# Kernel tuning notes

Measured on AMD Instinct MI355X. Metric: run time of the kernel, lower is better.

The kernel has to match this reference:

```python
import jax, jax.numpy as jnp
import numpy as np

N_OBJ, N_PTS, K_NN = 8, 2048, 10
TOL_CONTACT = 0.01


def setup_inputs() -> dict:
    key = jax.random.key(0)
    k1, k2, k3 = jax.random.split(key, 3)
    # per-object sampled points: xyz + (unit) normals
    pts = jax.random.normal(k1, (N_OBJ, N_PTS, 6), dtype=jnp.float32)
    nrm = pts[..., 3:6]
    nrm = nrm / jnp.linalg.norm(nrm, axis=-1, keepdims=True)
    points = jnp.concatenate([pts[..., :3], nrm], axis=-1)
    # near-identity rigid-ish transforms (keeps inverse well conditioned)
    T_est = jnp.eye(4, dtype=jnp.float32)[None] + 0.05 * jax.random.normal(k2, (N_OBJ, 4, 4), dtype=jnp.float32)
    T_plane = jnp.eye(4, dtype=jnp.float32) + 0.05 * jax.random.normal(k3, (4, 4), dtype=jnp.float32)
    return {"points": points, "T_est": T_est, "T_plane": T_plane, "k": K_NN}


def reference(points, T_est, T_plane, k):
    # points: [N, P, 6] (xyz, normal), T_est: [N, 4, 4], T_plane: [4, 4]
    N = points.shape[0]
    M = jnp.linalg.inv(T_plane) @ T_est                      # [N,4,4]
    xyz = points[..., :3]
    x = jnp.einsum('nij,npj->npi', M[:, :3, :3], xyz) + M[:, None, :3, 3]  # [N,P,3] points in plane frame
    z = x[..., 2]                                            # plane signed distance [N,P]
    nrm = points[..., 3:6]                                   # normals (untransformed, as in source)

    # all-pairs squared distances: d2[b,o,p,q] = ||x[b,p] - x[o,q]||^2
    sq = jnp.sum(x * x, axis=-1)                             # [N,P]
    d2 = sq[:, None, :, None] + sq[None, :, None, :] - 2.0 * jnp.einsum('bpd,oqd->bopq', x, x)
    neg_d2, idx = jax.lax.top_k(-d2, k)                      # [N,N,P,k], nearest k in object o for query (b,p)
    dist = jnp.sqrt(jnp.maximum(-neg_d2, 0.0))               # [N,N,P,k]

    # gather nearest points / normals from source object o
    o_idx = jnp.arange(N)[None, :, None, None]               # broadcast over [N,N,P,k]
    near = x[o_idx, idx]                                     # [N,N,P,k,3]
    near_n = nrm[o_idx, idx]                                 # [N,N,P,k,3]

    grad = near - x[:, None, :, None, :]                     # [N,N,P,k,3]
    grad = grad / jnp.linalg.norm(grad, axis=-1, keepdims=True)
    insides = jnp.sum(near_n * grad, axis=-1) > 0            # [N,N,P,k]
    inside = jnp.sum(insides, axis=-1) > k * 0.8             # [N,N,P]

    d0 = dist[..., 0]                                        # nearest distance [N,N,P]
    d0 = jnp.where(inside, -d0, d0)
    self_mask = jnp.eye(N, dtype=bool)[:, :, None]           # exclude o == b
    d0 = jnp.where(self_mask, jnp.inf, d0)
    sd_other = jnp.min(d0, axis=1)                           # [N,P] min over other objects

    signed_distance = jnp.minimum(z, sd_other)               # [N,P]
    intersects = signed_distance < -TOL_CONTACT
    return signed_distance, intersects
```

## Files before the change

kernel.cpp:

```cpp
#include <hip/hip_runtime.h>
#include <cfloat>
#include <math.h>

#define N_OBJ 8
#define N_PTS 2048
#define KNN   10
#define TOLC  0.01f
#define TPB   256
#define NW    4
#define QC    (N_PTS / NW)
#define PC    64
#define NCHUNK (N_PTS / PC)

__device__ __forceinline__ unsigned int enc_f(float f) {
    unsigned int u = __float_as_uint(f);
    return (u & 0x80000000u) ? ~u : (u | 0x80000000u);
}
__device__ __forceinline__ float dec_f(unsigned int e) {
    unsigned int u = (e & 0x80000000u) ? (e & 0x7fffffffu) : ~e;
    return __uint_as_float(u);
}

__global__ void k_transform(const float* __restrict__ pts,
                            const float* __restrict__ T_est,
                            const float* __restrict__ T_plane,
                            float4* __restrict__ P4g,
                            float4* __restrict__ N4g,
                            unsigned int* __restrict__ SD) {
    int gid = blockIdx.x * blockDim.x + threadIdx.x;
    if (gid >= N_OBJ * N_PTS) return;
    int b = gid >> 11;

    double m[16];
#pragma unroll
    for (int i = 0; i < 16; i++) m[i] = (double)T_plane[i];
    double inv[16];
    inv[0]  =  m[5]*m[10]*m[15] - m[5]*m[11]*m[14] - m[9]*m[6]*m[15] + m[9]*m[7]*m[14] + m[13]*m[6]*m[11] - m[13]*m[7]*m[10];
    inv[4]  = -m[4]*m[10]*m[15] + m[4]*m[11]*m[14] + m[8]*m[6]*m[15] - m[8]*m[7]*m[14] - m[12]*m[6]*m[11] + m[12]*m[7]*m[10];
    inv[8]  =  m[4]*m[9]*m[15]  - m[4]*m[11]*m[13] - m[8]*m[5]*m[15] + m[8]*m[7]*m[13] + m[12]*m[5]*m[11] - m[12]*m[7]*m[9];
    inv[12] = -m[4]*m[9]*m[14]  + m[4]*m[10]*m[13] + m[8]*m[5]*m[14] - m[8]*m[6]*m[13] - m[12]*m[5]*m[10] + m[12]*m[6]*m[9];
    inv[1]  = -m[1]*m[10]*m[15] + m[1]*m[11]*m[14] + m[9]*m[2]*m[15] - m[9]*m[3]*m[14] - m[13]*m[2]*m[11] + m[13]*m[3]*m[10];
    inv[5]  =  m[0]*m[10]*m[15] - m[0]*m[11]*m[14] - m[8]*m[2]*m[15] + m[8]*m[3]*m[14] + m[12]*m[2]*m[11] - m[12]*m[3]*m[10];
    inv[9]  = -m[0]*m[9]*m[15]  + m[0]*m[11]*m[13] + m[8]*m[1]*m[15] - m[8]*m[3]*m[13] - m[12]*m[1]*m[11] + m[12]*m[3]*m[9];
    inv[13] =  m[0]*m[9]*m[14]  - m[0]*m[10]*m[13] - m[8]*m[1]*m[14] + m[8]*m[2]*m[13] + m[12]*m[1]*m[10] - m[12]*m[2]*m[9];
    inv[2]  =  m[1]*m[6]*m[15]  - m[1]*m[7]*m[14]  - m[5]*m[2]*m[15] + m[5]*m[3]*m[14] + m[13]*m[2]*m[7]  - m[13]*m[3]*m[6];
    inv[6]  = -m[0]*m[6]*m[15]  + m[0]*m[7]*m[14]  + m[4]*m[2]*m[15] - m[4]*m[3]*m[14] - m[12]*m[2]*m[7]  + m[12]*m[3]*m[6];
    inv[10] =  m[0]*m[5]*m[15]  - m[0]*m[7]*m[13]  - m[4]*m[1]*m[15] + m[4]*m[3]*m[13] + m[12]*m[1]*m[7]  - m[12]*m[3]*m[5];
    inv[14] = -m[0]*m[5]*m[14]  + m[0]*m[6]*m[13]  + m[4]*m[1]*m[14] - m[4]*m[2]*m[13] - m[12]*m[1]*m[6]  + m[12]*m[2]*m[5];
    inv[3]  = -m[1]*m[6]*m[11]  + m[1]*m[7]*m[10]  + m[5]*m[2]*m[11] - m[5]*m[3]*m[10] - m[9]*m[2]*m[7]   + m[9]*m[3]*m[6];
    inv[7]  =  m[0]*m[6]*m[11]  - m[0]*m[7]*m[10]  - m[4]*m[2]*m[11] + m[4]*m[3]*m[10] + m[8]*m[2]*m[7]   - m[8]*m[3]*m[6];
    inv[11] = -m[0]*m[5]*m[11]  + m[0]*m[7]*m[9]   + m[4]*m[1]*m[11] - m[4]*m[3]*m[9]  - m[8]*m[1]*m[7]   + m[8]*m[3]*m[5];
    inv[15] =  m[0]*m[5]*m[10]  - m[0]*m[6]*m[9]   - m[4]*m[1]*m[10] + m[4]*m[2]*m[9]  + m[8]*m[1]*m[6]   - m[8]*m[2]*m[5];
    double det  = m[0]*inv[0] + m[1]*inv[4] + m[2]*inv[8] + m[3]*inv[12];
    double rdet = 1.0 / det;

    const float* Te = T_est + b * 16;
    double M[12];
#pragma unroll
    for (int i = 0; i < 3; i++)
#pragma unroll
        for (int j = 0; j < 4; j++) {
            double s = 0.0;
#pragma unroll
            for (int kk = 0; kk < 4; kk++) s += inv[i*4+kk] * rdet * (double)Te[kk*4+j];
            M[i*4+j] = s;
        }

    const float* pp = pts + (size_t)gid * 6;
    double px = pp[0], py = pp[1], pz = pp[2];
    float nx = pp[3], ny = pp[4], nz = pp[5];
    float x = (float)(M[0]*px + M[1]*py + M[2]*pz  + M[3]);
    float y = (float)(M[4]*px + M[5]*py + M[6]*pz  + M[7]);
    float z = (float)(M[8]*px + M[9]*py + M[10]*pz + M[11]);
    float sq = fmaf(x, x, fmaf(y, y, z * z));
    float w  = fmaf(nx, x, fmaf(ny, y, nz * z));
    P4g[gid] = make_float4(x, y, z, sq);
    N4g[gid] = make_float4(nx, ny, nz, w);
    SD[gid]  = enc_f(z);
}

#define QB(PX,PY,PZ,PW,NX,NY,NZ,NWW) \
  "v_mul_f32 %[t0], " PZ ", %[mz]\n" \
  "v_fma_f32 %[t0], %[my], " PY ", %[t0]\n" \
  "v_fma_f32 %[t0], %[mx], " PX ", %[t0]\n" \
  "v_add_f32 %[t0], " PW ", %[t0]\n" \
  "v_mul_f32 %[t1], " NZ ", %[gz]\n" \
  "v_fma_f32 %[t1], %[gy], " NY ", %[t1]\n" \
  "v_fma_f32 %[t1], %[gx], " NX ", %[t1]\n" \
  "v_add_f32 %[t1], " NWW ", %[t1]\n" \
  "v_and_b32 %[t0], -2, %[t0]\n" \
  "v_cmp_lt_f32 vcc, 0, %[t1]\n" \
  "v_cndmask_b32_e64 %[t1], 0, 1, vcc\n" \
  "v_or_b32 %[t0], %[t0], %[t1]\n" \
  "v_med3_f32 %[d9], %[d8], %[d9], %[t0]\n" \
  "v_med3_f32 %[d8], %[d7], %[d8], %[t0]\n" \
  "v_med3_f32 %[d7], %[d6], %[d7], %[t0]\n" \
  "v_med3_f32 %[d6], %[d5], %[d6], %[t0]\n" \
  "v_med3_f32 %[d5], %[d4], %[d5], %[t0]\n" \
  "v_med3_f32 %[d4], %[d3], %[d4], %[t0]\n" \
  "v_med3_f32 %[d3], %[d2], %[d3], %[t0]\n" \
  "v_med3_f32 %[d2], %[d1], %[d2], %[t0]\n" \
  "v_med3_f32 %[d1], %[d0], %[d1], %[t0]\n" \
  "v_min_f32 %[d0], %[d0], %[t0]\n"

__global__ void __launch_bounds__(TPB, 8) k_pairs(const float4* __restrict__ P4g,
                                                  const float4* __restrict__ N4g,
                                                  unsigned int* __restrict__ SD) {
    __shared__ float MRG[NW][PC][KNN + 1];

    int bx   = blockIdx.x;
    int pair = bx >> 5;
    int c64  = bx & (NCHUNK - 1);
    int b  = pair / 7;
    int oi = pair % 7;
    int o  = oi + (oi >= b ? 1 : 0);
    int tid  = threadIdx.x;
    int lane = tid & 63;
    int wu   = __builtin_amdgcn_readfirstlane(tid >> 6);
    int p    = c64 * PC + lane;

    float4 xp = P4g[b * N_PTS + p];
    float mx = -2.0f * xp.x, my = -2.0f * xp.y, mz = -2.0f * xp.z;
    float gx = -xp.x, gy = -xp.y, gz = -xp.z;

    const float4* Po = P4g + o * N_PTS + wu * QC;
    const float4* No = N4g + o * N_PTS + wu * QC;
    unsigned long long ap = (unsigned long long)(uintptr_t)Po;
    unsigned long long an = (unsigned long long)(uintptr_t)No;
    unsigned int bpl = (unsigned int)ap, bph = (unsigned int)(ap >> 32);
    unsigned int bnl = (unsigned int)an, bnh = (unsigned int)(an >> 32);

    const float FMAXE = __uint_as_float(0x7F7FFFFEu);
    float d0_ = FMAXE, d1_ = FMAXE, d2_ = FMAXE, d3_ = FMAXE, d4_ = FMAXE;
    float d5_ = FMAXE, d6_ = FMAXE, d7_ = FMAXE, d8_ = FMAXE, d9_ = FMAXE;
    float t0, t1;

    asm volatile(
        "s_mov_b32 s32, %[bpl]\n"
        "s_mov_b32 s33, %[bph]\n"
        "s_mov_b32 s34, %[bnl]\n"
        "s_mov_b32 s35, %[bnh]\n"
        "s_load_dwordx16 s[36:51], s[32:33], 0x0\n"
        "s_load_dwordx16 s[52:67], s[34:35], 0x0\n"
        "s_mov_b32 s30, 0\n"
        "Lkp%=:\n"
        "s_waitcnt lgkmcnt(0)\n"
        "s_load_dwordx16 s[68:83], s[32:33], 0x40\n"
        "s_load_dwordx16 s[84:99], s[34:35], 0x40\n"
        QB("s36","s37","s38","s39","s52","s53","s54","s55")
        QB("s40","s41","s42","s43","s56","s57","s58","s59")
        QB("s44","s45","s46","s47","s60","s61","s62","s63")
        QB("s48","s49","s50","s51","s64","s65","s66","s67")
        "s_waitcnt lgkmcnt(0)\n"
        "s_load_dwordx16 s[36:51], s[32:33], 0x80\n"
        "s_load_dwordx16 s[52:67], s[34:35], 0x80\n"
        QB("s68","s69","s70","s71","s84","s85","s86","s87")
        QB("s72","s73","s74","s75","s88","s89","s90","s91")
        QB("s76","s77","s78","s79","s92","s93","s94","s95")
        QB("s80","s81","s82","s83","s96","s97","s98","s99")
        "s_add_u32 s32, s32, 0x80\n"
        "s_addc_u32 s33, s33, 0\n"
        "s_add_u32 s34, s34, 0x80\n"
        "s_addc_u32 s35, s35, 0\n"
        "s_add_u32 s30, s30, 1\n"
        "s_cmp_lt_u32 s30, 64\n"
        "s_cbranch_scc1 Lkp%=\n"
        "s_waitcnt lgkmcnt(0)\n"
        : [d0]"+v"(d0_), [d1]"+v"(d1_), [d2]"+v"(d2_), [d3]"+v"(d3_),
          [d4]"+v"(d4_), [d5]"+v"(d5_), [d6]"+v"(d6_), [d7]"+v"(d7_),
          [d8]"+v"(d8_), [d9]"+v"(d9_), [t0]"=&v"(t0), [t1]"=&v"(t1)
        : [mx]"v"(mx), [my]"v"(my), [mz]"v"(mz),
          [gx]"v"(gx), [gy]"v"(gy), [gz]"v"(gz),
          [bpl]"s"(bpl), [bph]"s"(bph), [bnl]"s"(bnl), [bnh]"s"(bnh)
        : "s30","s31","s32","s33","s34","s35","s36","s37","s38","s39",
          "s40","s41","s42","s43","s44","s45","s46","s47","s48","s49",
          "s50","s51","s52","s53","s54","s55","s56","s57","s58","s59",
          "s60","s61","s62","s63","s64","s65","s66","s67","s68","s69",
          "s70","s71","s72","s73","s74","s75","s76","s77","s78","s79",
          "s80","s81","s82","s83","s84","s85","s86","s87","s88","s89",
          "s90","s91","s92","s93","s94","s95","s96","s97","s98","s99",
          "scc","vcc","memory");

    float td[KNN] = {d0_, d1_, d2_, d3_, d4_, d5_, d6_, d7_, d8_, d9_};

    if (wu > 0) {
#pragma unroll
        for (int j = 0; j < KNN; j++) MRG[wu][lane][j] = td[j];
    }
    __syncthreads();

    if (wu == 0) {
#pragma unroll
        for (int ww = 1; ww < NW; ww++) {
#pragma unroll
            for (int j = 0; j < KNN; j++) {
                float cp = MRG[ww][lane][j];
#pragma unroll
                for (int t = KNN - 1; t >= 1; --t)
                    td[t] = __builtin_amdgcn_fmed3f(td[t - 1], td[t], cp);
                td[0] = fminf(td[0], cp);
            }
        }

        int cnt = 0;
#pragma unroll
        for (int j = 0; j < KNN; j++) cnt += (int)(__float_as_uint(td[j]) & 1u);
        float d2 = __uint_as_float(__float_as_uint(td[0]) & 0xFFFFFFFEu) + xp.w;
        float d0 = sqrtf(fmaxf(d2, 0.0f));
        if (cnt > 8) d0 = -d0;
        atomicMin(&SD[b * N_PTS + p], enc_f(d0));
    }
}

__global__ void k_final(const unsigned int* __restrict__ SD,
                       float* __restrict__ out) {
    int gid = blockIdx.x * blockDim.x + threadIdx.x;
    if (gid >= N_OBJ * N_PTS) return;
    float sd = dec_f(SD[gid]);
    out[gid] = sd;
    out[N_OBJ * N_PTS + gid] = (sd < -TOLC) ? 1.0f : 0.0f;
}

extern "C" void kernel_launch(void* const* d_in, const int* in_sizes, int n_in,
                              void* d_out, int out_size, void* d_ws, size_t ws_size,
                              hipStream_t stream) {
    const float* pts     = (const float*)d_in[0];
    const float* T_est   = (const float*)d_in[1];
    const float* T_plane = (const float*)d_in[2];

    float4*       P4 = (float4*)d_ws;
    float4*       N4 = P4 + N_OBJ * N_PTS;
    unsigned int* SD = (unsigned int*)(N4 + N_OBJ * N_PTS);

    float* out = (float*)d_out;

    k_transform<<<(N_OBJ * N_PTS) / 256, 256, 0, stream>>>(pts, T_est, T_plane, P4, N4, SD);
    k_pairs<<<N_OBJ * (N_OBJ - 1) * NCHUNK, TPB, 0, stream>>>(P4, N4, SD);
    k_final<<<(N_OBJ * N_PTS) / 256, 256, 0, stream>>>(SD, out);
}
```

Baseline: 168.1 us.

## Stream candidate points via vector global loads with triple-buffered VGPR pipeline

Replaces scalar s_load_dwordx16 streaming of candidate points and normals with wave-uniform global_load_dwordx4 into a three-slot VGPR ring. Loads are issued two slots ahead and waited on with vmcnt, so memory latency overlaps the top-k compute. This uses 96 extra VGPRs, so launch bounds drop from 8 to 4 waves per SIMD, trading occupancy for deeper software pipelining and less scalar-cache pressure.

New measurement: 260.2 us. +54.8%, slower.

```diff
diff --git a/kernel.cpp b/kernel.cpp
--- a/kernel.cpp
+++ b/kernel.cpp
@@ -103,7 +103,40 @@
   "v_med3_f32 %[d1], %[d0], %[d1], %[t0]\n" \
   "v_min_f32 %[d0], %[d0], %[t0]\n"
 
-__global__ void __launch_bounds__(TPB, 8) k_pairs(const float4* __restrict__ P4g,
+#define LDSLOT(P0,P1,P2,P3,Q0,Q1,Q2,Q3,O0,O1,O2,O3) \
+  "global_load_dwordx4 " P0 ", %[vz], s[32:33] offset:" O0 "\n" \
+  "global_load_dwordx4 " P1 ", %[vz], s[32:33] offset:" O1 "\n" \
+  "global_load_dwordx4 " P2 ", %[vz], s[32:33] offset:" O2 "\n" \
+  "global_load_dwordx4 " P3 ", %[vz], s[32:33] offset:" O3 "\n" \
+  "global_load_dwordx4 " Q0 ", %[vz], s[34:35] offset:" O0 "\n" \
+  "global_load_dwordx4 " Q1 ", %[vz], s[34:35] offset:" O1 "\n" \
+  "global_load_dwordx4 " Q2 ", %[vz], s[34:35] offset:" O2 "\n" \
+  "global_load_dwordx4 " Q3 ", %[vz], s[34:35] offset:" O3 "\n"
+
+#define SLOT0_LD(O0,O1,O2,O3) LDSLOT("v[32:35]","v[36:39]","v[40:43]","v[44:47]", \
+                                     "v[48:51]","v[52:55]","v[56:59]","v[60:63]",O0,O1,O2,O3)
+#define SLOT1_LD(O0,O1,O2,O3) LDSLOT("v[64:67]","v[68:71]","v[72:75]","v[76:79]", \
+                                     "v[80:83]","v[84:87]","v[88:91]","v[92:95]",O0,O1,O2,O3)
+#define SLOT2_LD(O0,O1,O2,O3) LDSLOT("v[96:99]","v[100:103]","v[104:107]","v[108:111]", \
+                                     "v[112:115]","v[116:119]","v[120:123]","v[124:127]",O0,O1,O2,O3)
+
+#define SLOT0_QB \
+  QB("v32","v33","v34","v35","v48","v49","v50","v51") \
+  QB("v36","v37","v38","v39","v52","v53","v54","v55") \
+  QB("v40","v41","v42","v43","v56","v57","v58","v59") \
+  QB("v44","v45","v46","v47","v60","v61","v62","v63")
+#define SLOT1_QB \
+  QB("v64","v65","v66","v67","v80","v81","v82","v83") \
+  QB("v68","v69","v70","v71","v84","v85","v86","v87") \
+  QB("v72","v73","v74","v75","v88","v89","v90","v91") \
+  QB("v76","v77","v78","v79","v92","v93","v94","v95")
+#define SLOT2_QB \
+  QB("v96","v97","v98","v99","v112","v113","v114","v115") \
+  QB("v100","v101","v102","v103","v116","v117","v118","v119") \
+  QB("v104","v105","v106","v107","v120","v121","v122","v123") \
+  QB("v108","v109","v110","v111","v124","v125","v126","v127")
+
+__global__ void __launch_bounds__(TPB, 4) k_pairs(const float4* __restrict__ P4g,
                                                   const float4* __restrict__ N4g,
                                                   unsigned int* __restrict__ SD) {
     __shared__ float MRG[NW][PC][KNN + 1];
@@ -140,45 +173,50 @@
         "s_mov_b32 s33, %[bph]\n"
         "s_mov_b32 s34, %[bnl]\n"
         "s_mov_b32 s35, %[bnh]\n"
-        "s_load_dwordx16 s[36:51], s[32:33], 0x0\n"
-        "s_load_dwordx16 s[52:67], s[34:35], 0x0\n"
+        SLOT0_LD("0","16","32","48")
+        SLOT1_LD("64","80","96","112")
         "s_mov_b32 s30, 0\n"
         "Lkp%=:\n"
-        "s_waitcnt lgkmcnt(0)\n"
-        "s_load_dwordx16 s[68:83], s[32:33], 0x40\n"
-        "s_load_dwordx16 s[84:99], s[34:35], 0x40\n"
-        QB("s36","s37","s38","s39","s52","s53","s54","s55")
-        QB("s40","s41","s42","s43","s56","s57","s58","s59")
-        QB("s44","s45","s46","s47","s60","s61","s62","s63")
-        QB("s48","s49","s50","s51","s64","s65","s66","s67")
-        "s_waitcnt lgkmcnt(0)\n"
-        "s_load_dwordx16 s[36:51], s[32:33], 0x80\n"
-        "s_load_dwordx16 s[52:67], s[34:35], 0x80\n"
-        QB("s68","s69","s70","s71","s84","s85","s86","s87")
-        QB("s72","s73","s74","s75","s88","s89","s90","s91")
-        QB("s76","s77","s78","s79","s92","s93","s94","s95")
-        QB("s80","s81","s82","s83","s96","s97","s98","s99")
-        "s_add_u32 s32, s32, 0x80\n"
+        SLOT2_LD("128","144","160","176")
+        "s_waitcnt vmcnt(16)\n"
+        SLOT0_QB
+        SLOT0_LD("192","208","224","240")
+        "s_waitcnt vmcnt(16)\n"
+        SLOT1_QB
+        SLOT1_LD("256","272","288","304")
+        "s_waitcnt vmcnt(16)\n"
+        SLOT2_QB
+        "s_add_u32 s32, s32, 0xc0\n"
         "s_addc_u32 s33, s33, 0\n"
-        "s_add_u32 s34, s34, 0x80\n"
+        "s_add_u32 s34, s34, 0xc0\n"
         "s_addc_u32 s35, s35, 0\n"
         "s_add_u32 s30, s30, 1\n"
-        "s_cmp_lt_u32 s30, 64\n"
+        "s_cmp_lt_u32 s30, 42\n"
         "s_cbranch_scc1 Lkp%=\n"
-        "s_waitcnt lgkmcnt(0)\n"
+        "s_waitcnt vmcnt(8)\n"
+        SLOT0_QB
+        "s_waitcnt vmcnt(0)\n"
+        SLOT1_QB
         : [d0]"+v"(d0_), [d1]"+v"(d1_), [d2]"+v"(d2_), [d3]"+v"(d3_),
           [d4]"+v"(d4_), [d5]"+v"(d5_), [d6]"+v"(d6_), [d7]"+v"(d7_),
           [d8]"+v"(d8_), [d9]"+v"(d9_), [t0]"=&v"(t0), [t1]"=&v"(t1)
         : [mx]"v"(mx), [my]"v"(my), [mz]"v"(mz),
           [gx]"v"(gx), [gy]"v"(gy), [gz]"v"(gz),
+          [vz]"v"(0),
           [bpl]"s"(bpl), [bph]"s"(bph), [bnl]"s"(bnl), [bnh]"s"(bnh)
-        : "s30","s31","s32","s33","s34","s35","s36","s37","s38","s39",
-          "s40","s41","s42","s43","s44","s45","s46","s47","s48","s49",
-          "s50","s51","s52","s53","s54","s55","s56","s57","s58","s59",
-          "s60","s61","s62","s63","s64","s65","s66","s67","s68","s69",
-          "s70","s71","s72","s73","s74","s75","s76","s77","s78","s79",
-          "s80","s81","s82","s83","s84","s85","s86","s87","s88","s89",
-          "s90","s91","s92","s93","s94","s95","s96","s97","s98","s99",
+        : "s30","s32","s33","s34","s35",
+          "v32","v33","v34","v35","v36","v37","v38","v39",
+          "v40","v41","v42","v43","v44","v45","v46","v47",
+          "v48","v49","v50","v51","v52","v53","v54","v55",
+          "v56","v57","v58","v59","v60","v61","v62","v63",
+          "v64","v65","v66","v67","v68","v69","v70","v71",
+          "v72","v73","v74","v75","v76","v77","v78","v79",
+          "v80","v81","v82","v83","v84","v85","v86","v87",
+          "v88","v89","v90","v91","v92","v93","v94","v95",
+          "v96","v97","v98","v99","v100","v101","v102","v103",
+          "v104","v105","v106","v107","v108","v109","v110","v111",
+          "v112","v113","v114","v115","v116","v117","v118","v119",
+          "v120","v121","v122","v123","v124","v125","v126","v127",
           "scc","vcc","memory");
 
     float td[KNN] = {d0_, d1_, d2_, d3_, d4_, d5_, d6_, d7_, d8_, d9_};
```

## Stage source object positions in LDS and read via ds_read_b128

Applied to the files above, without the earlier changes.

Copies the source object's 2048 point positions into shared memory per block, then reads them with LDS vector loads (broadcast across the wave) while normals still stream through scalar loads. This halves scalar memory traffic in the inner loop and doubles the per-iteration batch. In exchange it adds a cooperative staging copy, an extra barrier, 32KB LDS per block, 64 clobbered VGPRs, and lowers launch bounds occupancy from 8 to 4 waves; LDS reads are also mixed under the same lgkmcnt waits.

New measurement: 164.9 us. Within noise of the previous version (-1.9%).

```diff
diff --git a/kernel.cpp b/kernel.cpp
--- a/kernel.cpp
+++ b/kernel.cpp
@@ -103,10 +103,48 @@
   "v_med3_f32 %[d1], %[d0], %[d1], %[t0]\n" \
   "v_min_f32 %[d0], %[d0], %[t0]\n"
 
-__global__ void __launch_bounds__(TPB, 8) k_pairs(const float4* __restrict__ P4g,
+#define DS8(V0,V1,V2,V3,V4,V5,V6,V7,O0,O1,O2,O3,O4,O5,O6,O7) \
+  "ds_read_b128 " V0 ", %[lb] offset:" O0 "\n" \
+  "ds_read_b128 " V1 ", %[lb] offset:" O1 "\n" \
+  "ds_read_b128 " V2 ", %[lb] offset:" O2 "\n" \
+  "ds_read_b128 " V3 ", %[lb] offset:" O3 "\n" \
+  "ds_read_b128 " V4 ", %[lb] offset:" O4 "\n" \
+  "ds_read_b128 " V5 ", %[lb] offset:" O5 "\n" \
+  "ds_read_b128 " V6 ", %[lb] offset:" O6 "\n" \
+  "ds_read_b128 " V7 ", %[lb] offset:" O7 "\n"
+
+#define DSA(O0,O1,O2,O3,O4,O5,O6,O7) \
+  DS8("v[32:35]","v[36:39]","v[40:43]","v[44:47]", \
+      "v[48:51]","v[52:55]","v[56:59]","v[60:63]",O0,O1,O2,O3,O4,O5,O6,O7)
+#define DSB(O0,O1,O2,O3,O4,O5,O6,O7) \
+  DS8("v[64:67]","v[68:71]","v[72:75]","v[76:79]", \
+      "v[80:83]","v[84:87]","v[88:91]","v[92:95]",O0,O1,O2,O3,O4,O5,O6,O7)
+
+#define QB_A \
+  QB("v32","v33","v34","v35","s36","s37","s38","s39") \
+  QB("v36","v37","v38","v39","s40","s41","s42","s43") \
+  QB("v40","v41","v42","v43","s44","s45","s46","s47") \
+  QB("v44","v45","v46","v47","s48","s49","s50","s51") \
+  QB("v48","v49","v50","v51","s52","s53","s54","s55") \
+  QB("v52","v53","v54","v55","s56","s57","s58","s59") \
+  QB("v56","v57","v58","v59","s60","s61","s62","s63") \
+  QB("v60","v61","v62","v63","s64","s65","s66","s67")
+#define QB_B \
+  QB("v64","v65","v66","v67","s68","s69","s70","s71") \
+  QB("v68","v69","v70","v71","s72","s73","s74","s75") \
+  QB("v72","v73","v74","v75","s76","s77","s78","s79") \
+  QB("v76","v77","v78","v79","s80","s81","s82","s83") \
+  QB("v80","v81","v82","v83","s84","s85","s86","s87") \
+  QB("v84","v85","v86","v87","s88","s89","s90","s91") \
+  QB("v88","v89","v90","v91","s92","s93","s94","s95") \
+  QB("v92","v93","v94","v95","s96","s97","s98","s99")
+
+__global__ void __launch_bounds__(TPB, 4) k_pairs(const float4* __restrict__ P4g,
                                                   const float4* __restrict__ N4g,
                                                   unsigned int* __restrict__ SD) {
-    __shared__ float MRG[NW][PC][KNN + 1];
+    __shared__ __align__(16) unsigned char shraw[N_PTS * sizeof(float4) + 768];
+    float4* Pq = (float4*)shraw;
+    float (*MRG)[PC][KNN + 1] = (float (*)[PC][KNN + 1])shraw;
 
     int bx   = blockIdx.x;
     int pair = bx >> 5;
@@ -119,70 +157,76 @@
     int wu   = __builtin_amdgcn_readfirstlane(tid >> 6);
     int p    = c64 * PC + lane;
 
+    for (int i = tid; i < N_PTS; i += TPB) Pq[i] = P4g[o * N_PTS + i];
+
     float4 xp = P4g[b * N_PTS + p];
     float mx = -2.0f * xp.x, my = -2.0f * xp.y, mz = -2.0f * xp.z;
     float gx = -xp.x, gy = -xp.y, gz = -xp.z;
 
-    const float4* Po = P4g + o * N_PTS + wu * QC;
     const float4* No = N4g + o * N_PTS + wu * QC;
-    unsigned long long ap = (unsigned long long)(uintptr_t)Po;
     unsigned long long an = (unsigned long long)(uintptr_t)No;
-    unsigned int bpl = (unsigned int)ap, bph = (unsigned int)(ap >> 32);
     unsigned int bnl = (unsigned int)an, bnh = (unsigned int)(an >> 32);
+    unsigned int lb = (unsigned int)(uintptr_t)(&Pq[wu * QC]);
 
     const float FMAXE = __uint_as_float(0x7F7FFFFEu);
     float d0_ = FMAXE, d1_ = FMAXE, d2_ = FMAXE, d3_ = FMAXE, d4_ = FMAXE;
     float d5_ = FMAXE, d6_ = FMAXE, d7_ = FMAXE, d8_ = FMAXE, d9_ = FMAXE;
     float t0, t1;
 
+    __syncthreads();
+
     asm volatile(
-        "s_mov_b32 s32, %[bpl]\n"
-        "s_mov_b32 s33, %[bph]\n"
-        "s_mov_b32 s34, %[bnl]\n"
-        "s_mov_b32 s35, %[bnh]\n"
+        "s_mov_b32 s32, %[bnl]\n"
+        "s_mov_b32 s33, %[bnh]\n"
         "s_load_dwordx16 s[36:51], s[32:33], 0x0\n"
-        "s_load_dwordx16 s[52:67], s[34:35], 0x0\n"
+        "s_load_dwordx16 s[52:67], s[32:33], 0x40\n"
+        DSA("0","16","32","48","64","80","96","112")
         "s_mov_b32 s30, 0\n"
         "Lkp%=:\n"
         "s_waitcnt lgkmcnt(0)\n"
-        "s_load_dwordx16 s[68:83], s[32:33], 0x40\n"
-        "s_load_dwordx16 s[84:99], s[34:35], 0x40\n"
-        QB("s36","s37","s38","s39","s52","s53","s54","s55")
-        QB("s40","s41","s42","s43","s56","s57","s58","s59")
-        QB("s44","s45","s46","s47","s60","s61","s62","s63")
-        QB("s48","s49","s50","s51","s64","s65","s66","s67")
+        "s_load_dwordx16 s[68:83], s[32:33], 0x80\n"
+        "s_load_dwordx16 s[84:99], s[32:33], 0xc0\n"
+        DSB("128","144","160","176","192","208","224","240")
+        QB_A
         "s_waitcnt lgkmcnt(0)\n"
-        "s_load_dwordx16 s[36:51], s[32:33], 0x80\n"
-        "s_load_dwordx16 s[52:67], s[34:35], 0x80\n"
-        QB("s68","s69","s70","s71","s84","s85","s86","s87")
-        QB("s72","s73","s74","s75","s88","s89","s90","s91")
-        QB("s76","s77","s78","s79","s92","s93","s94","s95")
-        QB("s80","s81","s82","s83","s96","s97","s98","s99")
-        "s_add_u32 s32, s32, 0x80\n"
+        "s_load_dwordx16 s[36:51], s[32:33], 0x100\n"
+        "s_load_dwordx16 s[52:67], s[32:33], 0x140\n"
+        DSA("256","272","288","304","320","336","352","368")
+        QB_B
+        "s_add_u32 s32, s32, 0x100\n"
         "s_addc_u32 s33, s33, 0\n"
-        "s_add_u32 s34, s34, 0x80\n"
-        "s_addc_u32 s35, s35, 0\n"
+        "v_add_u32 %[lb], 256, %[lb]\n"
         "s_add_u32 s30, s30, 1\n"
-        "s_cmp_lt_u32 s30, 64\n"
+        "s_cmp_lt_u32 s30, 32\n"
         "s_cbranch_scc1 Lkp%=\n"
         "s_waitcnt lgkmcnt(0)\n"
         : [d0]"+v"(d0_), [d1]"+v"(d1_), [d2]"+v"(d2_), [d3]"+v"(d3_),
           [d4]"+v"(d4_), [d5]"+v"(d5_), [d6]"+v"(d6_), [d7]"+v"(d7_),
-          [d8]"+v"(d8_), [d9]"+v"(d9_), [t0]"=&v"(t0), [t1]"=&v"(t1)
+          [d8]"+v"(d8_), [d9]"+v"(d9_), [t0]"=&v"(t0), [t1]"=&v"(t1),
+          [lb]"+v"(lb)
         : [mx]"v"(mx), [my]"v"(my), [mz]"v"(mz),
           [gx]"v"(gx), [gy]"v"(gy), [gz]"v"(gz),
-          [bpl]"s"(bpl), [bph]"s"(bph), [bnl]"s"(bnl), [bnh]"s"(bnh)
-        : "s30","s31","s32","s33","s34","s35","s36","s37","s38","s39",
+          [bnl]"s"(bnl), [bnh]"s"(bnh)
+        : "s30","s32","s33","s36","s37","s38","s39",
           "s40","s41","s42","s43","s44","s45","s46","s47","s48","s49",
           "s50","s51","s52","s53","s54","s55","s56","s57","s58","s59",
           "s60","s61","s62","s63","s64","s65","s66","s67","s68","s69",
           "s70","s71","s72","s73","s74","s75","s76","s77","s78","s79",
           "s80","s81","s82","s83","s84","s85","s86","s87","s88","s89",
           "s90","s91","s92","s93","s94","s95","s96","s97","s98","s99",
+          "v32","v33","v34","v35","v36","v37","v38","v39",
+          "v40","v41","v42","v43","v44","v45","v46","v47",
+          "v48","v49","v50","v51","v52","v53","v54","v55",
+          "v56","v57","v58","v59","v60","v61","v62","v63",
+          "v64","v65","v66","v67","v68","v69","v70","v71",
+          "v72","v73","v74","v75","v76","v77","v78","v79",
+          "v80","v81","v82","v83","v84","v85","v86","v87",
+          "v88","v89","v90","v91","v92","v93","v94","v95",
           "scc","vcc","memory");
 
     float td[KNN] = {d0_, d1_, d2_, d3_, d4_, d5_, d6_, d7_, d8_, d9_};
 
+    __syncthreads();
     if (wu > 0) {
 #pragma unroll
         for (int j = 0; j < KNN; j++) MRG[wu][lane][j] = td[j];
```

## Fuse transform, pair kNN and finalize into one cooperative persistent kernel

Applied to the files above, without the earlier changes.

Combines the three kernel launches into a single cooperative kernel that uses grid-wide syncs between the transform, pair-tile kNN and output phases. Blocks loop persistently over pair tiles, and the grid size is set from occupancy and CU count. The aim is to remove the launch overhead and inter-kernel gaps between the three launches. In exchange it adds grid-sync cost, drops launch bounds from 8 to 7 blocks per CU, which may lower occupancy, and keeps the multi-kernel path as a fallback.

Measured after the change: 474.7 us. 2.82x slower.

```diff
diff --git a/kernel.cpp b/kernel.cpp
--- a/kernel.cpp
+++ b/kernel.cpp
@@ -1,6 +1,9 @@
 #include <hip/hip_runtime.h>
+#include <hip/hip_cooperative_groups.h>
 #include <cfloat>
 #include <math.h>
+
+namespace cg = cooperative_groups;
 
 #define N_OBJ 8
 #define N_PTS 2048
@@ -11,6 +14,7 @@
 #define QC    (N_PTS / NW)
 #define PC    64
 #define NCHUNK (N_PTS / PC)
+#define NTILES (N_OBJ * (N_OBJ - 1) * NCHUNK)
 
 __device__ __forceinline__ unsigned int enc_f(float f) {
     unsigned int u = __float_as_uint(f);
@@ -21,14 +25,10 @@
     return __uint_as_float(u);
 }
 
-__global__ void k_transform(const float* __restrict__ pts,
-                            const float* __restrict__ T_est,
-                            const float* __restrict__ T_plane,
-                            float4* __restrict__ P4g,
-                            float4* __restrict__ N4g,
-                            unsigned int* __restrict__ SD) {
-    int gid = blockIdx.x * blockDim.x + threadIdx.x;
-    if (gid >= N_OBJ * N_PTS) return;
+__device__ __forceinline__ void transform_point(
+        int gid, const float* __restrict__ pts, const float* __restrict__ T_est,
+        const float* __restrict__ T_plane, float4* __restrict__ P4g,
+        float4* __restrict__ N4g, unsigned int* __restrict__ SD) {
     int b = gid >> 11;
 
     double m[16];
@@ -103,20 +103,15 @@
   "v_med3_f32 %[d1], %[d0], %[d1], %[t0]\n" \
   "v_min_f32 %[d0], %[d0], %[t0]\n"
 
-__global__ void __launch_bounds__(TPB, 8) k_pairs(const float4* __restrict__ P4g,
-                                                  const float4* __restrict__ N4g,
-                                                  unsigned int* __restrict__ SD) {
-    __shared__ float MRG[NW][PC][KNN + 1];
-
-    int bx   = blockIdx.x;
-    int pair = bx >> 5;
-    int c64  = bx & (NCHUNK - 1);
+__device__ __forceinline__ void pair_tile(
+        int t, const float4* __restrict__ P4g, const float4* __restrict__ N4g,
+        unsigned int* __restrict__ SD, float (*MRG)[PC][KNN + 1],
+        int tid, int lane, int wu) {
+    int pair = t >> 5;
+    int c64  = t & (NCHUNK - 1);
     int b  = pair / 7;
     int oi = pair % 7;
     int o  = oi + (oi >= b ? 1 : 0);
-    int tid  = threadIdx.x;
-    int lane = tid & 63;
-    int wu   = __builtin_amdgcn_readfirstlane(tid >> 6);
     int p    = c64 * PC + lane;
 
     float4 xp = P4g[b * N_PTS + p];
@@ -196,8 +191,8 @@
             for (int j = 0; j < KNN; j++) {
                 float cp = MRG[ww][lane][j];
 #pragma unroll
-                for (int t = KNN - 1; t >= 1; --t)
-                    td[t] = __builtin_amdgcn_fmed3f(td[t - 1], td[t], cp);
+                for (int tt = KNN - 1; tt >= 1; --tt)
+                    td[tt] = __builtin_amdgcn_fmed3f(td[tt - 1], td[tt], cp);
                 td[0] = fminf(td[0], cp);
             }
         }
@@ -210,10 +205,69 @@
         if (cnt > 8) d0 = -d0;
         atomicMin(&SD[b * N_PTS + p], enc_f(d0));
     }
+    __syncthreads();
+}
+
+__global__ void __launch_bounds__(TPB, 7) k_fused(
+        const float* __restrict__ pts, const float* __restrict__ T_est,
+        const float* __restrict__ T_plane, float4* __restrict__ P4g,
+        float4* __restrict__ N4g, unsigned int* __restrict__ SD,
+        float* __restrict__ out) {
+    __shared__ float MRG[NW][PC][KNN + 1];
+    cg::grid_group grid = cg::this_grid();
+
+    int tid  = threadIdx.x;
+    int bx   = blockIdx.x;
+    int lane = tid & 63;
+    int wu   = __builtin_amdgcn_readfirstlane(tid >> 6);
+
+    {
+        int i = tid * gridDim.x + bx;
+        if (i < N_OBJ * N_PTS)
+            transform_point(i, pts, T_est, T_plane, P4g, N4g, SD);
+    }
+    __threadfence();
+    grid.sync();
+
+    for (int t = bx; t < NTILES; t += gridDim.x)
+        pair_tile(t, P4g, N4g, SD, MRG, tid, lane, wu);
+
+    __threadfence();
+    grid.sync();
+
+    {
+        int gid = bx * TPB + tid;
+        if (gid < N_OBJ * N_PTS) {
+            float sd = dec_f(SD[gid]);
+            out[gid] = sd;
+            out[N_OBJ * N_PTS + gid] = (sd < -TOLC) ? 1.0f : 0.0f;
+        }
+    }
+}
+
+__global__ void k_transform(const float* __restrict__ pts,
+                            const float* __restrict__ T_est,
+                            const float* __restrict__ T_plane,
+                            float4* __restrict__ P4g,
+                            float4* __restrict__ N4g,
+                            unsigned int* __restrict__ SD) {
+    int gid = blockIdx.x * blockDim.x + threadIdx.x;
+    if (gid >= N_OBJ * N_PTS) return;
+    transform_point(gid, pts, T_est, T_plane, P4g, N4g, SD);
+}
+
+__global__ void __launch_bounds__(TPB, 7) k_pairs(const float4* __restrict__ P4g,
+                                                  const float4* __restrict__ N4g,
+                                                  unsigned int* __restrict__ SD) {
+    __shared__ float MRG[NW][PC][KNN + 1];
+    int tid  = threadIdx.x;
+    int lane = tid & 63;
+    int wu   = __builtin_amdgcn_readfirstlane(tid >> 6);
+    pair_tile(blockIdx.x, P4g, N4g, SD, MRG, tid, lane, wu);
 }
 
 __global__ void k_final(const unsigned int* __restrict__ SD,
-                       float* __restrict__ out) {
+                        float* __restrict__ out) {
     int gid = blockIdx.x * blockDim.x + threadIdx.x;
     if (gid >= N_OBJ * N_PTS) return;
     float sd = dec_f(SD[gid]);
@@ -231,10 +285,35 @@
     float4*       P4 = (float4*)d_ws;
     float4*       N4 = P4 + N_OBJ * N_PTS;
     unsigned int* SD = (unsigned int*)(N4 + N_OBJ * N_PTS);
-
-    float* out = (float*)d_out;
-
-    k_transform<<<(N_OBJ * N_PTS) / 256, 256, 0, stream>>>(pts, T_est, T_plane, P4, N4, SD);
-    k_pairs<<<N_OBJ * (N_OBJ - 1) * NCHUNK, TPB, 0, stream>>>(P4, N4, SD);
-    k_final<<<(N_OBJ * N_PTS) / 256, 256, 0, stream>>>(SD, out);
-}
+    float*        out = (float*)d_out;
+
+    static int nblk = -2;
+    if (nblk == -2) {
+        int dev = 0, coop = 0, ncu = 0, maxB = 0;
+        (void)hipGetDevice(&dev);
+        (void)hipDeviceGetAttribute(&coop, hipDeviceAttributeCooperativeLaunch, dev);
+        (void)hipDeviceGetAttribute(&ncu, hipDeviceAttributeMultiprocessorCount, dev);
+        hipError_t oe = hipOccupancyMaxActiveBlocksPerMultiprocessor(
+                            &maxB, (const void*)k_fused, TPB, 0);
+        if (coop && oe == hipSuccess && maxB > 0 && ncu > 0) {
+            long cap = (long)maxB * (long)ncu;
+            nblk = (int)(cap < (long)NTILES ? cap : (long)NTILES);
+        } else {
+            nblk = -1;
+        }
+    }
+
+    if (nblk > 0) {
+        void* args[] = {(void*)&pts, (void*)&T_est, (void*)&T_plane,
+                        (void*)&P4, (void*)&N4, (void*)&SD, (void*)&out};
+        hipError_t err = hipLaunchCooperativeKernel(
+            (const void*)k_fused, dim3(nblk), dim3(TPB), args, 0, stream);
+        if (err == hipSuccess) return;
+        (void)hipGetLastError();
+        nblk = -1;
+    }
+
+    k_transform<<<(N_OBJ * N_PTS) / TPB, TPB, 0, stream>>>(pts, T_est, T_plane, P4, N4, SD);
+    k_pairs<<<NTILES, TPB, 0, stream>>>(P4, N4, SD);
+    k_final<<<(N_OBJ * N_PTS) / TPB, TPB, 0, stream>>>(SD, out);
+}
```
